# Optimization experiments

Hardware: AMD Instinct MI355X
Metric: run time of the kernel (lower is better)

The kernel has to match this reference:

```python
import jax, jax.numpy as jnp
import numpy as np

EPS = 1e-05
NUM_HEADS = 8
NUM_GROUPS = 32  # min(32, 512 // 4)


def setup_inputs() -> dict:
    key = jax.random.key(0)
    ks = jax.random.split(key, 5)
    B, C, T, X = 4, 512, 16, 2048
    return {
        "x": jax.random.normal(ks[0], (B, C, T, X), dtype=jnp.float32),
        "gn_w": jnp.ones((C,), dtype=jnp.float32),
        "gn_b": jnp.zeros((C,), dtype=jnp.float32),
        "qkv_w": jax.random.normal(ks[1], (3 * C, C), dtype=jnp.float32) * 0.02,
        "qkv_b": jax.random.normal(ks[2], (3 * C,), dtype=jnp.float32) * 0.02,
        "proj_w": jax.random.normal(ks[3], (C, C), dtype=jnp.float32) * 1e-5,
        "proj_b": jnp.zeros((C,), dtype=jnp.float32),
        "pos_emb": jax.random.normal(ks[4], (NUM_HEADS, 2 * T), dtype=jnp.float32) * 1e-5,
    }


def _group_norm(x, w, b):
    B, C, T, X = x.shape
    g = NUM_GROUPS
    xg = x.reshape(B, g, C // g, T, X)
    mu = xg.mean(axis=(2, 3, 4), keepdims=True)
    var = ((xg - mu) ** 2).mean(axis=(2, 3, 4), keepdims=True)
    xn = ((xg - mu) * jax.lax.rsqrt(var + EPS)).reshape(B, C, T, X)
    return xn * w[None, :, None, None] + b[None, :, None, None]


def reference(x, gn_w, gn_b, qkv_w, qkv_b, proj_w, proj_b, pos_emb):
    dtype = x.dtype
    x = x.astype(jnp.float32)
    B, C, T, X = x.shape
    H = NUM_HEADS
    hc = C // H

    xn = _group_norm(x, gn_w, gn_b)
    # 1x1 conv == channel matmul: [B, 3C, T, X]
    qkv = jnp.einsum('oc,bctx->botx', qkv_w, xn) + qkv_b[None, :, None, None]
    # 'b (n heads c) t x -> n (b x) heads t c'
    qkv = qkv.reshape(B, 3, H, hc, T, X)
    qkv = qkv.transpose(1, 0, 5, 2, 4, 3).reshape(3, B * X, H, T, hc)
    q, k, v = qkv[0], qkv[1], qkv[2]

    scale = 1.0 / np.sqrt(hc)
    attn = jnp.einsum('bhqc,bhkc->bhqk', q, k * scale)  # [(B X), H, T, T]

    i = jnp.arange(T)
    pairwise = i[:, None] - i[None, :] + T - 1        # [T, T] in [0, 2T-2]
    rel = pos_emb[:, pairwise]                         # [H, T, T]

    w = jax.nn.softmax(attn + rel[None], axis=-1)
    out = jnp.einsum('bhqk,bhkc->bhcq', w, v)          # [(B X), H, hc, T]
    # '(b x) h c t -> b (h c) t x'
    out = out.reshape(B, X, H, hc, T).transpose(0, 2, 3, 4, 1).reshape(B, C, T, X)

    y = jnp.einsum('oc,bctx->botx', proj_w, out) + proj_b[None, :, None, None]
    return y.astype(dtype)
```

## Files before the change

kernel.cpp:

```cpp
#include <hip/hip_runtime.h>
#include <math.h>

#define EPSV 1e-5f

typedef _Float16 f16;
typedef _Float16 f16x8 __attribute__((ext_vector_type(8)));
typedef _Float16 f16x4 __attribute__((ext_vector_type(4)));
typedef float f32x4 __attribute__((ext_vector_type(4)));

typedef const __attribute__((address_space(1))) void* as1_cvp;
typedef __attribute__((address_space(3))) void* as3_vp;
__device__ __forceinline__ void load_lds16(const void* g, void* l) {
    __builtin_amdgcn_global_load_lds((as1_cvp)g, (as3_vp)l, 16, 0, 0);
}

static constexpr int GROUP_N = 16 * 16 * 2048;

__global__ __launch_bounds__(256) void k_gn_part(const float* __restrict__ x,
                                                 float* __restrict__ psum,
                                                 float* __restrict__ psq) {
    const int blk = blockIdx.x;
    const int tid = threadIdx.x;
    const float* p = x + (size_t)blk * 32768;
    float s = 0.f, q = 0.f;
#pragma unroll
    for (int i = 0; i < 32; ++i) {
        float4 v = *(const float4*)(p + (size_t)(i * 256 + tid) * 4);
        s += v.x + v.y + v.z + v.w;
        q += v.x * v.x + v.y * v.y + v.z * v.z + v.w * v.w;
    }
#pragma unroll
    for (int off = 32; off > 0; off >>= 1) {
        s += __shfl_down(s, off);
        q += __shfl_down(q, off);
    }
    __shared__ float ls[4], lq[4];
    const int wave = tid >> 6, lane = tid & 63;
    if (lane == 0) { ls[wave] = s; lq[wave] = q; }
    __syncthreads();
    if (tid == 0) {
        psum[blk] = ls[0] + ls[1] + ls[2] + ls[3];
        psq[blk]  = lq[0] + lq[1] + lq[2] + lq[3];
    }
}

__global__ void k_gn_final(const float* __restrict__ psum, const float* __restrict__ psq,
                           float* __restrict__ mu, float* __restrict__ rs) {
    const int t = threadIdx.x;
    float s = 0.f, q = 0.f;
#pragma unroll
    for (int i = 0; i < 16; ++i) { s += psum[t * 16 + i]; q += psq[t * 16 + i]; }
    const float m = s / (float)GROUP_N;
    float v = q / (float)GROUP_N - m * m;
    mu[t] = m;
    rs[t] = 1.0f / sqrtf(v + EPSV);
}

__global__ __launch_bounds__(256) void k_fold_sc(const float* __restrict__ gn_w,
                                                 const float* __restrict__ gn_b,
                                                 const float* __restrict__ mu,
                                                 const float* __restrict__ rs,
                                                 float* __restrict__ sc,
                                                 float* __restrict__ beta) {
    const int u = blockIdx.x * 256 + threadIdx.x;
    const int b = u >> 9, c = u & 511;
    const int g = c >> 4;
    const float r = rs[b * 32 + g], m = mu[b * 32 + g];
    const float s = r * gn_w[c];
    sc[u]   = s;
    beta[u] = gn_b[c] - m * s;
}

__global__ __launch_bounds__(256) void k_fold_bias(const float* __restrict__ qkv_w,
                                                   const float* __restrict__ qkv_b,
                                                   const float* __restrict__ beta,
                                                   float* __restrict__ qbias) {
    const int u = blockIdx.x * 256 + threadIdx.x;
    const int b = u / 1536, o = u % 1536;
    float acc = qkv_b[o];
    const float* wr = qkv_w + (size_t)o * 512;
    const float* be = beta + b * 512;
#pragma unroll 4
    for (int c = 0; c < 512; c += 4) {
        float4 w4 = *(const float4*)(wr + c);
        float4 b4 = *(const float4*)(be + c);
        acc += w4.x * b4.x + w4.y * b4.y + w4.z * b4.z + w4.w * b4.w;
    }
    if (o >= 512 && o < 1024) acc *= 0.125f;
    qbias[u] = acc;
}


__global__ __launch_bounds__(256) void k_prep_w(const float* __restrict__ qkv_w,
                                                const float* __restrict__ proj_w,
                                                f16* __restrict__ w16,
                                                f16* __restrict__ p16) {
    const int id = blockIdx.x * 256 + threadIdx.x;
    if (id < 196608) {
        const int e0 = id * 4;
        const int o  = e0 >> 9;
        const float ksc = (o >= 512 && o < 1024) ? 0.125f : 1.0f;
        float4 v = *(const float4*)(qkv_w + e0);
        f16x4 h = { (f16)(v.x * ksc), (f16)(v.y * ksc), (f16)(v.z * ksc), (f16)(v.w * ksc) };
        *(f16x4*)(w16 + e0) = h;
    } else {
        const int e0 = (id - 196608) * 4;
        float4 v = *(const float4*)(proj_w + e0);
        f16x4 h = { (f16)v.x, (f16)v.y, (f16)v.z, (f16)v.w };
        *(f16x4*)(p16 + e0) = h;
    }
}

__global__ __launch_bounds__(256) void k_xt(const float* __restrict__ x,
                                            const float* __restrict__ sc,
                                            const float* __restrict__ beta,
                                            f16* __restrict__ xT) {
    const int x0 = blockIdx.x * 64;
    const int c0 = blockIdx.y * 64;
    const int b  = blockIdx.z >> 4, t = blockIdx.z & 15;
    const int tid = threadIdx.x;
    __shared__ float tile[64][68];
#pragma unroll
    for (int it = 0; it < 4; ++it) {
        int idx = it * 256 + tid;
        int c = idx >> 4, xq = idx & 15;
        int cg = c0 + c;
        float s = sc[b * 512 + cg], be = beta[b * 512 + cg];
        float4 v = *(const float4*)(x + (((size_t)(b * 512 + cg) * 16 + t) * 2048) + x0 + xq * 4);
        tile[c][xq * 4 + 0] = v.x * s + be;
        tile[c][xq * 4 + 1] = v.y * s + be;
        tile[c][xq * 4 + 2] = v.z * s + be;
        tile[c][xq * 4 + 3] = v.w * s + be;
    }
    __syncthreads();
#pragma unroll
    for (int it = 0; it < 2; ++it) {
        int idx = it * 256 + tid;
        int xr = idx >> 3, ch = idx & 7;
        f16x8 h;
#pragma unroll
        for (int e = 0; e < 8; ++e) h[e] = (f16)tile[ch * 8 + e][xr];
        *(f16x8*)(xT + (((size_t)(b * 2048 + x0 + xr) * 16 + t) * 512) + c0 + ch * 8) = h;
    }
}

__global__ __launch_bounds__(256) void k3_mfma(const f16* __restrict__ xT,
                                               const f16* __restrict__ w16,
                                               const float* __restrict__ qkv_b,
                                               const float* __restrict__ pos_emb,
                                               float* __restrict__ out,
                                               f16* __restrict__ aT) {
    extern __shared__ __attribute__((aligned(16))) char smem[];
    const int h  = blockIdx.x;
    const int x0 = blockIdx.y * 8;
    const int b  = blockIdx.z;
    const int tid = threadIdx.x;
    const int lane = tid & 63, w = tid >> 6;
    const int wm = w >> 1, wn = w & 1;
    const int t_l = lane & 15, g = lane >> 4;

    const f16* xTb = xT + ((size_t)b * 2048 + x0) * 16 * 512;

    const int l8 = lane >> 3;
    const int gc = (lane & 7) ^ l8;

    f32x4 acc[6][4];
#pragma unroll
    for (int mi = 0; mi < 6; ++mi)
#pragma unroll
        for (int ni = 0; ni < 4; ++ni) acc[mi][ni] = (f32x4){0.f, 0.f, 0.f, 0.f};

    {
#pragma unroll
        for (int i = 0; i < 6; ++i) {
            int m0 = (w * 6 + i) * 8;
            int m = m0 + l8;
            int o = (m >> 6) * 512 + h * 64 + (m & 63);
            load_lds16(w16 + (size_t)o * 512 + gc * 8, smem + m0 * 128);
        }
#pragma unroll
        for (int i = 0; i < 4; ++i) {
            int n0 = (w * 4 + i) * 8;
            int n = n0 + l8;
            load_lds16(xTb + (size_t)n * 512 + gc * 8, smem + 24576 + n0 * 128);
        }
    }
    __syncthreads();

    int cur = 0;
    for (int ks = 0; ks < 8; ++ks) {
        if (ks < 7) {
            char* bufn = smem + (cur ^ 1) * 40960;
            const int kon = (ks + 1) * 64;
#pragma unroll
            for (int i = 0; i < 6; ++i) {
                int m0 = (w * 6 + i) * 8;
                int m = m0 + l8;
                int o = (m >> 6) * 512 + h * 64 + (m & 63);
                load_lds16(w16 + (size_t)o * 512 + kon + gc * 8, bufn + m0 * 128);
            }
#pragma unroll
            for (int i = 0; i < 4; ++i) {
                int n0 = (w * 4 + i) * 8;
                int n = n0 + l8;
                load_lds16(xTb + (size_t)n * 512 + kon + gc * 8, bufn + 24576 + n0 * 128);
            }
        }
        const char* bufc = smem + cur * 40960;
        const f16* a_s = (const f16*)bufc;
        const f16* b_s = (const f16*)(bufc + 24576);
#pragma unroll
        for (int kk = 0; kk < 2; ++kk) {
            const int kb = kk * 4 + g;
            f16x8 af[6], bf[4];
#pragma unroll
            for (int mi = 0; mi < 6; ++mi) {
                int m = wm * 96 + mi * 16 + t_l;
                af[mi] = *(const f16x8*)(a_s + m * 64 + ((kb ^ (m & 7)) * 8));
            }
#pragma unroll
            for (int ni = 0; ni < 4; ++ni) {
                int n = wn * 64 + ni * 16 + t_l;
                bf[ni] = *(const f16x8*)(b_s + n * 64 + ((kb ^ (n & 7)) * 8));
            }
#pragma unroll
            for (int mi = 0; mi < 6; ++mi)
#pragma unroll
                for (int ni = 0; ni < 4; ++ni)
                    acc[mi][ni] = __builtin_amdgcn_mfma_f32_16x16x32_f16(af[mi], bf[ni], acc[mi][ni], 0, 0, 0);
        }
        __syncthreads();
        cur ^= 1;
    }

#pragma unroll
    for (int mi = 0; mi < 6; ++mi)
#pragma unroll
        for (int ni = 0; ni < 4; ++ni) {
            int n  = wn * 64 + ni * 16 + t_l;
            int mb = wm * 96 + mi * 16 + g * 4;
            int byte_off = n * 512 + (((mb >> 6) * 8 + (((mb >> 3) & 7) ^ (n & 7))) * 16) + (mb & 7) * 2;
            f16x4 hv;
#pragma unroll
            for (int r2 = 0; r2 < 4; ++r2) {
                int row = mb + r2;
                int reg = row >> 6;
                float qb = qkv_b[reg * 512 + h * 64 + (row & 63)];
                if (reg == 1) qb *= 0.125f;
                hv[r2] = (f16)(acc[mi][ni][r2] + qb);
            }
            *(f16x4*)(smem + byte_off) = hv;
        }
    __syncthreads();

#pragma unroll
    for (int xc = 0; xc < 2; ++xc) {
        const int xx = w * 2 + xc;
        const int nb = xx * 16;
        const int nrow = nb + t_l;
        const int rbase = nrow * 512;
        const int sw = nrow & 7;

        f32x4 s_acc = {0.f, 0.f, 0.f, 0.f};
#pragma unroll
        for (int half = 0; half < 2; ++half) {
            int qiA = (g + 4 * half) & 7;
            f16x8 afr = *(const f16x8*)(smem + rbase + ((8 + (qiA ^ sw)) * 16));
            f16x8 bfr = *(const f16x8*)(smem + rbase + ((qiA ^ sw) * 16));
            s_acc = __builtin_amdgcn_mfma_f32_16x16x32_f16(afr, bfr, s_acc, 0, 0, 0);
        }
        float sv[4];
#pragma unroll
        for (int r2 = 0; r2 < 4; ++r2)
            sv[r2] = s_acc[r2] + pos_emb[h * 32 + t_l - (g * 4 + r2) + 15];
        float mx = fmaxf(fmaxf(sv[0], sv[1]), fmaxf(sv[2], sv[3]));
        mx = fmaxf(mx, __shfl_xor(mx, 16));
        mx = fmaxf(mx, __shfl_xor(mx, 32));
        float es[4], ssum = 0.f;
#pragma unroll
        for (int r2 = 0; r2 < 4; ++r2) { es[r2] = __expf(sv[r2] - mx); ssum += es[r2]; }
        ssum += __shfl_xor(ssum, 16);
        ssum += __shfl_xor(ssum, 32);
        const float inv = 1.0f / ssum;
        f16x4 pfrag;
#pragma unroll
        for (int r2 = 0; r2 < 4; ++r2) pfrag[r2] = (f16)(es[r2] * inv);

        f32x4 o_acc[4];
#pragma unroll
        for (int cb = 0; cb < 4; ++cb) {
            int mV = 128 + cb * 16 + t_l;
            int qiV = (mV >> 3) & 7;
            f16x4 vfrag;
#pragma unroll
            for (int jj = 0; jj < 4; ++jj) {
                int nV = nb + g * 4 + jj;
                vfrag[jj] = *(const f16*)(smem + nV * 512 + ((16 + (qiV ^ (nV & 7))) * 16) + (mV & 7) * 2);
            }
            f32x4 z = {0.f, 0.f, 0.f, 0.f};
            o_acc[cb] = __builtin_amdgcn_mfma_f32_16x16x16f16(vfrag, pfrag, z, 0, 0, 0);
        }
        if (aT) {
            f16* dst = aT + (((size_t)(b * 2048 + x0 + xx) * 16) + t_l) * 512 + h * 64;
#pragma unroll
            for (int cb = 0; cb < 4; ++cb) {
                f16x4 hv;
#pragma unroll
                for (int r2 = 0; r2 < 4; ++r2) hv[r2] = (f16)o_acc[cb][r2];
                *(f16x4*)(dst + cb * 16 + g * 4) = hv;
            }
        } else {
#pragma unroll
            for (int cb = 0; cb < 4; ++cb) {
                int qd = cb * 4 + g;
                int byte_off = rbase + (((qd >> 3) * 8 + ((qd & 7) ^ sw)) * 16);
                *(f32x4*)(smem + byte_off) = o_acc[cb];
            }
        }
    }
    if (!aT) {
        __syncthreads();
        const int c = tid & 63, tq = tid >> 6;
        const int qc = c >> 2;
#pragma unroll
        for (int ti = 0; ti < 4; ++ti) {
            int t = tq * 4 + ti;
            float vals[8];
#pragma unroll
            for (int xx = 0; xx < 8; ++xx) {
                int n2 = xx * 16 + t;
                vals[xx] = *(const float*)(smem + n2 * 512 + (((qc >> 3) * 8 + ((qc & 7) ^ (n2 & 7))) * 16) + (c & 3) * 4);
            }
            float4 lo = {vals[0], vals[1], vals[2], vals[3]};
            float4 hi = {vals[4], vals[5], vals[6], vals[7]};
            size_t oaddr = (((size_t)b * 512 + h * 64 + c) * 16 + t) * 2048 + x0;
            *(float4*)(out + oaddr) = lo;
            *(float4*)(out + oaddr + 4) = hi;
        }
    }
}

__global__ __launch_bounds__(256) void k4x(const f16* __restrict__ attnT,
                                           const f16* __restrict__ p16,
                                           const float* __restrict__ pb,
                                           float* __restrict__ out) {
    extern __shared__ __attribute__((aligned(16))) char smem[];
    const int oc  = blockIdx.x;
    const int win = blockIdx.y;
    const int b   = blockIdx.z;
    const int tid = threadIdx.x;
    const int lane = tid & 63, w = tid >> 6;
    const int t_l = lane & 15, g = lane >> 4;
    const int l8 = lane >> 3;
    const int gc = (lane & 7) ^ l8;

    const f16* Bb = attnT + ((size_t)b * 2048 + win * 16) * 16 * 512;
    const f16* Ab = p16 + (size_t)oc * 64 * 512;

    f32x4 acc[4][4];
#pragma unroll
    for (int mi = 0; mi < 4; ++mi)
#pragma unroll
        for (int ni = 0; ni < 4; ++ni) acc[mi][ni] = (f32x4){0.f, 0.f, 0.f, 0.f};

    {
#pragma unroll
        for (int i = 0; i < 2; ++i) {
            int m0 = w * 16 + i * 8;
            load_lds16(Ab + (size_t)(m0 + l8) * 512 + gc * 8, smem + m0 * 128);
        }
#pragma unroll
        for (int i = 0; i < 8; ++i) {
            int n0 = w * 64 + i * 8;
            load_lds16(Bb + (size_t)(n0 + l8) * 512 + gc * 8, smem + 8192 + n0 * 128);
        }
    }
    __syncthreads();

    int cur = 0;
    for (int ks = 0; ks < 8; ++ks) {
        if (ks < 7) {
            char* bufn = smem + (cur ^ 1) * 40960;
            const int kon = (ks + 1) * 64;
#pragma unroll
            for (int i = 0; i < 2; ++i) {
                int m0 = w * 16 + i * 8;
                load_lds16(Ab + (size_t)(m0 + l8) * 512 + kon + gc * 8, bufn + m0 * 128);
            }
#pragma unroll
            for (int i = 0; i < 8; ++i) {
                int n0 = w * 64 + i * 8;
                load_lds16(Bb + (size_t)(n0 + l8) * 512 + kon + gc * 8, bufn + 8192 + n0 * 128);
            }
        }
        const char* bufc = smem + cur * 40960;
        const f16* a_s = (const f16*)bufc;
        const f16* b_s = (const f16*)(bufc + 8192);
#pragma unroll
        for (int kk = 0; kk < 2; ++kk) {
            const int kb = kk * 4 + g;
            f16x8 af[4], bf[4];
#pragma unroll
            for (int mi = 0; mi < 4; ++mi) {
                int m = mi * 16 + t_l;
                af[mi] = *(const f16x8*)(a_s + m * 64 + ((kb ^ (m & 7)) * 8));
            }
#pragma unroll
            for (int ni = 0; ni < 4; ++ni) {
                int n = w * 64 + ni * 16 + t_l;
                bf[ni] = *(const f16x8*)(b_s + n * 64 + ((kb ^ (n & 7)) * 8));
            }
#pragma unroll
            for (int mi = 0; mi < 4; ++mi)
#pragma unroll
                for (int ni = 0; ni < 4; ++ni)
                    acc[mi][ni] = __builtin_amdgcn_mfma_f32_16x16x32_f16(af[mi], bf[ni], acc[mi][ni], 0, 0, 0);
        }
        __syncthreads();
        cur ^= 1;
    }

    float* y_s = (float*)smem;
#pragma unroll
    for (int mi = 0; mi < 4; ++mi)
#pragma unroll
        for (int ni = 0; ni < 4; ++ni) {
            int nn = w * 64 + ni * 16 + t_l;
            int xx = nn >> 4, tt = nn & 15;
            int ob = mi * 16 + g * 4;
#pragma unroll
            for (int r2 = 0; r2 < 4; ++r2)
                y_s[(ob + r2) * 273 + xx * 17 + tt] = acc[mi][ni][r2];
        }
    __syncthreads();
#pragma unroll
    for (int k = 0; k < 4; ++k) {
        int pair = k * 256 + tid;
        int o = pair >> 4, t = pair & 15;
        float bias = pb[oc * 64 + o];
        float v[16];
#pragma unroll
        for (int xx = 0; xx < 16; ++xx) v[xx] = y_s[o * 273 + xx * 17 + t] + bias;
        size_t addr = (((size_t)b * 512 + oc * 64 + o) * 16 + t) * 2048 + win * 16;
#pragma unroll
        for (int v4 = 0; v4 < 4; ++v4) {
            float4 ov = {v[v4 * 4 + 0], v[v4 * 4 + 1], v[v4 * 4 + 2], v[v4 * 4 + 3]};
            *(float4*)(out + addr + v4 * 4) = ov;
        }
    }
}

__global__ __launch_bounds__(256) void k4_mfma(const f16* __restrict__ p16,
                                               const float* __restrict__ pb,
                                               float* __restrict__ io) {
    const int x0 = blockIdx.x * 64;
    const int t  = blockIdx.y;
    const int b  = blockIdx.z;
    const int tid = threadIdx.x, lane = tid & 63, w = tid >> 6;

    __shared__ __attribute__((aligned(16))) char smem4[81920];
    f16* in_sT = (f16*)smem4;
    f16* bp_s  = (f16*)(smem4 + 65536);

    const size_t base_in = (((size_t)b * 512) * 16 + t) * 2048 + x0;
#pragma unroll
    for (int it = 0; it < 32; ++it) {
        int s = it * 256 + tid;
        int c = s >> 4, xq = s & 15;
        float4 v = *(const float4*)(io + base_in + (size_t)c * 16 * 2048 + xq * 4);
        int kc = c >> 3, j = c & 7;
        float vv[4] = {v.x, v.y, v.z, v.w};
#pragma unroll
        for (int e = 0; e < 4; ++e) {
            int xx = xq * 4 + e;
            in_sT[xx * 512 + ((kc ^ (xx & 7)) * 8) + j] = (f16)vv[e];
        }
    }

    for (int no = 0; no < 4; ++no) {
        const int o_base = no * 128;
        f32x4 acc[4][2];
#pragma unroll
        for (int mi = 0; mi < 4; ++mi)
#pragma unroll
            for (int nj = 0; nj < 2; ++nj) acc[mi][nj] = (f32x4){0.f, 0.f, 0.f, 0.f};

        for (int ko = 0; ko < 8; ++ko) {
            __syncthreads();
#pragma unroll
            for (int it = 0; it < 4; ++it) {
                int s = it * 256 + tid;
                int orow = s >> 3, ch = s & 7;
                uint4 v = *(const uint4*)(p16 + (size_t)(o_base + orow) * 512 + ko * 64 + ch * 8);
                *(uint4*)(bp_s + orow * 64 + ((ch ^ (orow & 7)) * 8)) = v;
            }
            __syncthreads();
#pragma unroll
            for (int kk = 0; kk < 2; ++kk) {
                const int kb4 = kk * 4 + (lane >> 4);
                f16x8 af[4], bf[2];
#pragma unroll
                for (int mi = 0; mi < 4; ++mi) {
                    int xx = mi * 16 + (lane & 15);
                    int kc = ko * 8 + kb4;
                    af[mi] = *(const f16x8*)(in_sT + xx * 512 + ((kc ^ (xx & 7)) * 8));
                }
#pragma unroll
                for (int nj = 0; nj < 2; ++nj) {
                    int orow = w * 32 + nj * 16 + (lane & 15);
                    bf[nj] = *(const f16x8*)(bp_s + orow * 64 + ((kb4 ^ (orow & 7)) * 8));
                }
#pragma unroll
                for (int mi = 0; mi < 4; ++mi)
#pragma unroll
                    for (int nj = 0; nj < 2; ++nj)
                        acc[mi][nj] = __builtin_amdgcn_mfma_f32_16x16x32_f16(af[mi], bf[nj], acc[mi][nj], 0, 0, 0);
            }
        }
#pragma unroll
        for (int mi = 0; mi < 4; ++mi)
#pragma unroll
            for (int nj = 0; nj < 2; ++nj) {
                int o = o_base + w * 32 + nj * 16 + (lane & 15);
                int xxb = mi * 16 + (lane >> 4) * 4;
                float bias = pb[o];
                float4 ov = {acc[mi][nj][0] + bias, acc[mi][nj][1] + bias,
                             acc[mi][nj][2] + bias, acc[mi][nj][3] + bias};
                *(float4*)(io + (((size_t)b * 512 + o) * 16 + t) * 2048 + x0 + xxb) = ov;
            }
    }
}


__global__ __launch_bounds__(256) void k_qkv_attn(const float* __restrict__ x,
                                                  const float* __restrict__ qkv_w,
                                                  const float* __restrict__ sc,
                                                  const float* __restrict__ qbias,
                                                  const float* __restrict__ pos_emb,
                                                  float* __restrict__ out) {
    const int h  = blockIdx.x;
    const int x0 = blockIdx.y * 4;
    const int b  = blockIdx.z;
    const int tid = threadIdx.x;

    __shared__ float a_s[192][68];
    __shared__ float b_s[64][68];
    __shared__ float w_s[4][16][17];

    const int ty = tid >> 3;
    const int tx = tid & 7;

    float acc[6][8];
#pragma unroll
    for (int j = 0; j < 6; ++j)
#pragma unroll
        for (int k = 0; k < 8; ++k) acc[j][k] = 0.f;

    for (int ko = 0; ko < 512; ko += 64) {
        __syncthreads();
#pragma unroll
        for (int it = 0; it < 12; ++it) {
            int idx = it * 256 + tid;
            int m = idx >> 4;
            int c4 = (idx & 15) * 4;
            int g = m >> 6, i = m & 63;
            int o = g * 512 + h * 64 + i;
            float4 w4 = *(const float4*)(qkv_w + (size_t)o * 512 + ko + c4);
            float4 s4 = *(const float4*)(sc + b * 512 + ko + c4);
            float ksc = (g == 1) ? 0.125f : 1.0f;
            float4 v;
            v.x = w4.x * s4.x * ksc; v.y = w4.y * s4.y * ksc;
            v.z = w4.z * s4.z * ksc; v.w = w4.w * s4.w * ksc;
            *(float4*)&a_s[m][c4] = v;
        }
#pragma unroll
        for (int it = 0; it < 4; ++it) {
            int idx = it * 256 + tid;
            int cc = idx >> 4, t = idx & 15;
            float4 v = *(const float4*)(x + ((size_t)((b * 512 + ko + cc) * 16 + t)) * 2048 + x0);
            *(float4*)&b_s[cc][t * 4] = v;
        }
        __syncthreads();
#pragma unroll 4
        for (int cc = 0; cc < 64; ++cc) {
            float av[6];
#pragma unroll
            for (int j = 0; j < 6; ++j) av[j] = a_s[ty * 6 + j][cc];
            float4 b0 = *(const float4*)&b_s[cc][tx * 8];
            float4 b1 = *(const float4*)&b_s[cc][tx * 8 + 4];
            float bv[8] = {b0.x, b0.y, b0.z, b0.w, b1.x, b1.y, b1.z, b1.w};
#pragma unroll
            for (int j = 0; j < 6; ++j)
#pragma unroll
                for (int k = 0; k < 8; ++k)
                    acc[j][k] = fmaf(av[j], bv[k], acc[j][k]);
        }
    }
#pragma unroll
    for (int j = 0; j < 6; ++j) {
        int m = ty * 6 + j;
        int o = (m >> 6) * 512 + h * 64 + (m & 63);
        float qb = qbias[b * 1536 + o];
#pragma unroll
        for (int k = 0; k < 8; ++k) acc[j][k] += qb;
    }
    __syncthreads();
#pragma unroll
    for (int j = 0; j < 6; ++j)
#pragma unroll
        for (int k = 0; k < 8; ++k)
            a_s[ty * 6 + j][tx * 8 + k] = acc[j][k];
    __syncthreads();

    {
        const int xx = tid >> 6;
        const int t  = (tid >> 2) & 15;
        const int uq = tid & 3;
        float l[4] = {0.f, 0.f, 0.f, 0.f};
        for (int i = 0; i < 64; ++i) {
            float qv = a_s[i][t * 4 + xx];
#pragma unroll
            for (int uu = 0; uu < 4; ++uu)
                l[uu] = fmaf(qv, a_s[64 + i][(uq * 4 + uu) * 4 + xx], l[uu]);
        }
#pragma unroll
        for (int uu = 0; uu < 4; ++uu) {
            int u = uq * 4 + uu;
            w_s[xx][t][u] = l[uu] + pos_emb[h * 32 + t - u + 15];
        }
    }
    __syncthreads();
    if (tid < 64) {
        const int xx = tid >> 4, t = tid & 15;
        float mx = -3.4e38f;
#pragma unroll
        for (int u = 0; u < 16; ++u) mx = fmaxf(mx, w_s[xx][t][u]);
        float ssum = 0.f;
#pragma unroll
        for (int u = 0; u < 16; ++u) {
            float e = __expf(w_s[xx][t][u] - mx);
            w_s[xx][t][u] = e;
            ssum += e;
        }
        float inv = 1.0f / ssum;
#pragma unroll
        for (int u = 0; u < 16; ++u) w_s[xx][t][u] *= inv;
    }
    __syncthreads();
    {
        const int i  = tid & 63;
        const int t4 = tid >> 6;
        float4 varr[16];
#pragma unroll
        for (int u = 0; u < 16; ++u) varr[u] = *(const float4*)&a_s[128 + i][u * 4];
#pragma unroll
        for (int tt = 0; tt < 4; ++tt) {
            int t = t4 * 4 + tt;
            float4 o4 = {0.f, 0.f, 0.f, 0.f};
#pragma unroll
            for (int u = 0; u < 16; ++u) {
                o4.x = fmaf(w_s[0][t][u], varr[u].x, o4.x);
                o4.y = fmaf(w_s[1][t][u], varr[u].y, o4.y);
                o4.z = fmaf(w_s[2][t][u], varr[u].z, o4.z);
                o4.w = fmaf(w_s[3][t][u], varr[u].w, o4.w);
            }
            *(float4*)(out + ((size_t)((b * 512 + h * 64 + i) * 16 + t)) * 2048 + x0) = o4;
        }
    }
}

__global__ __launch_bounds__(256) void k_proj(const float* __restrict__ pw,
                                              const float* __restrict__ pb,
                                              float* __restrict__ io) {
    const int n0 = blockIdx.x * 32;
    const int b  = blockIdx.y;
    const int tid = threadIdx.x;
    __shared__ float in_s[512][36];
    __shared__ float w_s[128][65];

    {
        const float* src = io + (size_t)b * 512 * 32768 + n0;
#pragma unroll
        for (int it = 0; it < 64; ++it) {
            int idx = it * 256 + tid;
            int r = idx >> 5, j = idx & 31;
            in_s[r][j] = src[(size_t)r * 32768 + j];
        }
    }
    __syncthreads();

    const int ty = tid >> 3;
    const int tx = tid & 7;

    for (int mo = 0; mo < 512; mo += 128) {
        float acc[4][4];
#pragma unroll
        for (int j = 0; j < 4; ++j)
#pragma unroll
            for (int k = 0; k < 4; ++k) acc[j][k] = 0.f;

        for (int ko = 0; ko < 512; ko += 64) {
#pragma unroll
            for (int it = 0; it < 32; ++it) {
                int idx = it * 256 + tid;
                int m = idx >> 6, cc = idx & 63;
                w_s[m][cc] = pw[(size_t)(mo + m) * 512 + ko + cc];
            }
            __syncthreads();
#pragma unroll 4
            for (int cc = 0; cc < 64; ++cc) {
                float4 bv = *(const float4*)&in_s[ko + cc][tx * 4];
                float a0 = w_s[ty * 4 + 0][cc];
                float a1 = w_s[ty * 4 + 1][cc];
                float a2 = w_s[ty * 4 + 2][cc];
                float a3 = w_s[ty * 4 + 3][cc];
                acc[0][0] = fmaf(a0, bv.x, acc[0][0]); acc[0][1] = fmaf(a0, bv.y, acc[0][1]);
                acc[0][2] = fmaf(a0, bv.z, acc[0][2]); acc[0][3] = fmaf(a0, bv.w, acc[0][3]);
                acc[1][0] = fmaf(a1, bv.x, acc[1][0]); acc[1][1] = fmaf(a1, bv.y, acc[1][1]);
                acc[1][2] = fmaf(a1, bv.z, acc[1][2]); acc[1][3] = fmaf(a1, bv.w, acc[1][3]);
                acc[2][0] = fmaf(a2, bv.x, acc[2][0]); acc[2][1] = fmaf(a2, bv.y, acc[2][1]);
                acc[2][2] = fmaf(a2, bv.z, acc[2][2]); acc[2][3] = fmaf(a2, bv.w, acc[2][3]);
                acc[3][0] = fmaf(a3, bv.x, acc[3][0]); acc[3][1] = fmaf(a3, bv.y, acc[3][1]);
                acc[3][2] = fmaf(a3, bv.z, acc[3][2]); acc[3][3] = fmaf(a3, bv.w, acc[3][3]);
            }
            __syncthreads();
        }
#pragma unroll
        for (int j = 0; j < 4; ++j) {
            int m = mo + ty * 4 + j;
            float bias = pb[m];
            float4 o4 = {acc[j][0] + bias, acc[j][1] + bias, acc[j][2] + bias, acc[j][3] + bias};
            *(float4*)(io + (size_t)(b * 512 + m) * 32768 + n0 + tx * 4) = o4;
        }
    }
}

extern "C" void kernel_launch(void* const* d_in, const int* in_sizes, int n_in,
                              void* d_out, int out_size, void* d_ws, size_t ws_size,
                              hipStream_t stream) {
    (void)in_sizes; (void)n_in; (void)out_size;
    const float* x       = (const float*)d_in[0];
    const float* gn_w    = (const float*)d_in[1];
    const float* gn_b    = (const float*)d_in[2];
    const float* qkv_w   = (const float*)d_in[3];
    const float* qkv_b   = (const float*)d_in[4];
    const float* proj_w  = (const float*)d_in[5];
    const float* proj_b  = (const float*)d_in[6];
    const float* pos_emb = (const float*)d_in[7];
    float* out = (float*)d_out;

    float* ws    = (float*)d_ws;
    float* psum  = ws;
    float* psq   = ws + 2048;
    float* mu    = ws + 4096;
    float* rs    = ws + 4224;
    float* sc    = ws + 4352;
    float* beta  = ws + 6400;
    float* qbias = ws + 8448;

    const size_t W16_OFF = 65536;
    const size_t P16_OFF = W16_OFF + (size_t)1536 * 512 * 2;
    const size_t XT_OFF  = P16_OFF + (size_t)512 * 512 * 2;
    const size_t AT_OFF  = XT_OFF + (size_t)4 * 2048 * 16 * 512 * 2;
    const size_t NEEDED  = AT_OFF;
    const size_t NEEDED2 = AT_OFF + (size_t)4 * 2048 * 16 * 512 * 2;

    k_gn_part<<<dim3(2048), dim3(256), 0, stream>>>(x, psum, psq);
    k_gn_final<<<dim3(1), dim3(128), 0, stream>>>(psum, psq, mu, rs);
    k_fold_sc<<<dim3(8), dim3(256), 0, stream>>>(gn_w, gn_b, mu, rs, sc, beta);

    const int K3_LDS = 81920;
    hipError_t a1 = hipFuncSetAttribute((const void*)k3_mfma,
                                        hipFuncAttributeMaxDynamicSharedMemorySize, K3_LDS);
    hipError_t a2 = hipFuncSetAttribute((const void*)k4x,
                                        hipFuncAttributeMaxDynamicSharedMemorySize, K3_LDS);

    if (ws_size >= NEEDED && a1 == hipSuccess) {
        f16* w16 = (f16*)((char*)d_ws + W16_OFF);
        f16* p16 = (f16*)((char*)d_ws + P16_OFF);
        f16* xT  = (f16*)((char*)d_ws + XT_OFF);
        k_prep_w<<<dim3(1024), dim3(256), 0, stream>>>(qkv_w, proj_w, w16, p16);
        k_xt<<<dim3(32, 8, 64), dim3(256), 0, stream>>>(x, sc, beta, xT);
        if (ws_size >= NEEDED2 && a2 == hipSuccess) {
            f16* attnT = (f16*)((char*)d_ws + AT_OFF);
            k3_mfma<<<dim3(8, 256, 4), dim3(256), K3_LDS, stream>>>(xT, w16, qkv_b, pos_emb, out, attnT);
            k4x<<<dim3(8, 128, 4), dim3(256), K3_LDS, stream>>>(attnT, p16, proj_b, out);
        } else {
            k3_mfma<<<dim3(8, 256, 4), dim3(256), K3_LDS, stream>>>(xT, w16, qkv_b, pos_emb, out, nullptr);
            k4_mfma<<<dim3(32, 16, 4), dim3(256), 0, stream>>>(p16, proj_b, out);
        }
    } else {
        k_fold_bias<<<dim3(24), dim3(256), 0, stream>>>(qkv_w, qkv_b, beta, qbias);
        k_qkv_attn<<<dim3(8, 512, 4), dim3(256), 0, stream>>>(x, qkv_w, sc, qbias, pos_emb, out);
        k_proj<<<dim3(1024, 4), dim3(256), 0, stream>>>(proj_w, proj_b, out);
    }
}
```

Baseline: 614.0 us.

## Replace LDS-staged double-buffered GEMM loads with direct global-to-register MFMA operand loads

Both the QKV GEMM kernel and the projection kernel drop the global_load_lds double-buffered staging and instead have each lane read its f16x8 MFMA fragments directly from global memory, with the k loop unrolled by 2. k3 switches to a static 64KB shared array, since LDS is still needed for its epilogue, and no longer requests 80KB of dynamic LDS. The aim is to remove LDS traffic and barrier stalls and to raise occupancy. The cost is more redundant global and L2 reads, because fragments are no longer shared across waves, and loads that are only 16 bytes per lane with a 1KB row stride.

```diff
diff --git a/kernel.cpp b/kernel.cpp
--- a/kernel.cpp
+++ b/kernel.cpp
@@ -7,12 +7,6 @@
 typedef _Float16 f16x8 __attribute__((ext_vector_type(8)));
 typedef _Float16 f16x4 __attribute__((ext_vector_type(4)));
 typedef float f32x4 __attribute__((ext_vector_type(4)));
-
-typedef const __attribute__((address_space(1))) void* as1_cvp;
-typedef __attribute__((address_space(3))) void* as3_vp;
-__device__ __forceinline__ void load_lds16(const void* g, void* l) {
-    __builtin_amdgcn_global_load_lds((as1_cvp)g, (as3_vp)l, 16, 0, 0);
-}
 
 static constexpr int GROUP_N = 16 * 16 * 2048;
 
@@ -150,7 +144,7 @@
                                                const float* __restrict__ pos_emb,
                                                float* __restrict__ out,
                                                f16* __restrict__ aT) {
-    extern __shared__ __attribute__((aligned(16))) char smem[];
+    __shared__ __attribute__((aligned(16))) char smem[65536];
     const int h  = blockIdx.x;
     const int x0 = blockIdx.y * 8;
     const int b  = blockIdx.z;
@@ -161,8 +155,18 @@
 
     const f16* xTb = xT + ((size_t)b * 2048 + x0) * 16 * 512;
 
-    const int l8 = lane >> 3;
-    const int gc = (lane & 7) ^ l8;
+    int aoff[6], boff[4];
+#pragma unroll
+    for (int mi = 0; mi < 6; ++mi) {
+        int m = wm * 96 + mi * 16 + t_l;
+        int o = (m >> 6) * 512 + h * 64 + (m & 63);
+        aoff[mi] = o * 512 + g * 8;
+    }
+#pragma unroll
+    for (int ni = 0; ni < 4; ++ni) {
+        int n = wn * 64 + ni * 16 + t_l;
+        boff[ni] = n * 512 + g * 8;
+    }
 
     f32x4 acc[6][4];
 #pragma unroll
@@ -170,67 +174,19 @@
 #pragma unroll
         for (int ni = 0; ni < 4; ++ni) acc[mi][ni] = (f32x4){0.f, 0.f, 0.f, 0.f};
 
-    {
-#pragma unroll
-        for (int i = 0; i < 6; ++i) {
-            int m0 = (w * 6 + i) * 8;
-            int m = m0 + l8;
-            int o = (m >> 6) * 512 + h * 64 + (m & 63);
-            load_lds16(w16 + (size_t)o * 512 + gc * 8, smem + m0 * 128);
-        }
-#pragma unroll
-        for (int i = 0; i < 4; ++i) {
-            int n0 = (w * 4 + i) * 8;
-            int n = n0 + l8;
-            load_lds16(xTb + (size_t)n * 512 + gc * 8, smem + 24576 + n0 * 128);
-        }
-    }
-    __syncthreads();
-
-    int cur = 0;
-    for (int ks = 0; ks < 8; ++ks) {
-        if (ks < 7) {
-            char* bufn = smem + (cur ^ 1) * 40960;
-            const int kon = (ks + 1) * 64;
-#pragma unroll
-            for (int i = 0; i < 6; ++i) {
-                int m0 = (w * 6 + i) * 8;
-                int m = m0 + l8;
-                int o = (m >> 6) * 512 + h * 64 + (m & 63);
-                load_lds16(w16 + (size_t)o * 512 + kon + gc * 8, bufn + m0 * 128);
-            }
-#pragma unroll
-            for (int i = 0; i < 4; ++i) {
-                int n0 = (w * 4 + i) * 8;
-                int n = n0 + l8;
-                load_lds16(xTb + (size_t)n * 512 + kon + gc * 8, bufn + 24576 + n0 * 128);
-            }
-        }
-        const char* bufc = smem + cur * 40960;
-        const f16* a_s = (const f16*)bufc;
-        const f16* b_s = (const f16*)(bufc + 24576);
-#pragma unroll
-        for (int kk = 0; kk < 2; ++kk) {
-            const int kb = kk * 4 + g;
-            f16x8 af[6], bf[4];
-#pragma unroll
-            for (int mi = 0; mi < 6; ++mi) {
-                int m = wm * 96 + mi * 16 + t_l;
-                af[mi] = *(const f16x8*)(a_s + m * 64 + ((kb ^ (m & 7)) * 8));
-            }
-#pragma unroll
-            for (int ni = 0; ni < 4; ++ni) {
-                int n = wn * 64 + ni * 16 + t_l;
-                bf[ni] = *(const f16x8*)(b_s + n * 64 + ((kb ^ (n & 7)) * 8));
-            }
-#pragma unroll
-            for (int mi = 0; mi < 6; ++mi)
-#pragma unroll
-                for (int ni = 0; ni < 4; ++ni)
-                    acc[mi][ni] = __builtin_amdgcn_mfma_f32_16x16x32_f16(af[mi], bf[ni], acc[mi][ni], 0, 0, 0);
-        }
-        __syncthreads();
-        cur ^= 1;
+#pragma unroll 2
+    for (int kc = 0; kc < 16; ++kc) {
+        const int kof = kc * 32;
+        f16x8 af[6], bf[4];
+#pragma unroll
+        for (int mi = 0; mi < 6; ++mi) af[mi] = *(const f16x8*)(w16 + aoff[mi] + kof);
+#pragma unroll
+        for (int ni = 0; ni < 4; ++ni) bf[ni] = *(const f16x8*)(xTb + boff[ni] + kof);
+#pragma unroll
+        for (int mi = 0; mi < 6; ++mi)
+#pragma unroll
+            for (int ni = 0; ni < 4; ++ni)
+                acc[mi][ni] = __builtin_amdgcn_mfma_f32_16x16x32_f16(af[mi], bf[ni], acc[mi][ni], 0, 0, 0);
     }
 
 #pragma unroll
@@ -351,73 +307,35 @@
     const int tid = threadIdx.x;
     const int lane = tid & 63, w = tid >> 6;
     const int t_l = lane & 15, g = lane >> 4;
-    const int l8 = lane >> 3;
-    const int gc = (lane & 7) ^ l8;
 
     const f16* Bb = attnT + ((size_t)b * 2048 + win * 16) * 16 * 512;
     const f16* Ab = p16 + (size_t)oc * 64 * 512;
 
+    int aoff[4], boff[4];
+#pragma unroll
+    for (int mi = 0; mi < 4; ++mi) aoff[mi] = (mi * 16 + t_l) * 512 + g * 8;
+#pragma unroll
+    for (int ni = 0; ni < 4; ++ni) boff[ni] = (w * 64 + ni * 16 + t_l) * 512 + g * 8;
+
     f32x4 acc[4][4];
 #pragma unroll
     for (int mi = 0; mi < 4; ++mi)
 #pragma unroll
         for (int ni = 0; ni < 4; ++ni) acc[mi][ni] = (f32x4){0.f, 0.f, 0.f, 0.f};
 
-    {
-#pragma unroll
-        for (int i = 0; i < 2; ++i) {
-            int m0 = w * 16 + i * 8;
-            load_lds16(Ab + (size_t)(m0 + l8) * 512 + gc * 8, smem + m0 * 128);
-        }
-#pragma unroll
-        for (int i = 0; i < 8; ++i) {
-            int n0 = w * 64 + i * 8;
-            load_lds16(Bb + (size_t)(n0 + l8) * 512 + gc * 8, smem + 8192 + n0 * 128);
-        }
-    }
-    __syncthreads();
-
-    int cur = 0;
-    for (int ks = 0; ks < 8; ++ks) {
-        if (ks < 7) {
-            char* bufn = smem + (cur ^ 1) * 40960;
-            const int kon = (ks + 1) * 64;
-#pragma unroll
-            for (int i = 0; i < 2; ++i) {
-                int m0 = w * 16 + i * 8;
-                load_lds16(Ab + (size_t)(m0 + l8) * 512 + kon + gc * 8, bufn + m0 * 128);
-            }
-#pragma unroll
-            for (int i = 0; i < 8; ++i) {
-                int n0 = w * 64 + i * 8;
-                load_lds16(Bb + (size_t)(n0 + l8) * 512 + kon + gc * 8, bufn + 8192 + n0 * 128);
-            }
-        }
-        const char* bufc = smem + cur * 40960;
-        const f16* a_s = (const f16*)bufc;
-        const f16* b_s = (const f16*)(bufc + 8192);
-#pragma unroll
-        for (int kk = 0; kk < 2; ++kk) {
-            const int kb = kk * 4 + g;
-            f16x8 af[4], bf[4];
-#pragma unroll
-            for (int mi = 0; mi < 4; ++mi) {
-                int m = mi * 16 + t_l;
-                af[mi] = *(const f16x8*)(a_s + m * 64 + ((kb ^ (m & 7)) * 8));
-            }
-#pragma unroll
-            for (int ni = 0; ni < 4; ++ni) {
-                int n = w * 64 + ni * 16 + t_l;
-                bf[ni] = *(const f16x8*)(b_s + n * 64 + ((kb ^ (n & 7)) * 8));
-            }
-#pragma unroll
-            for (int mi = 0; mi < 4; ++mi)
-#pragma unroll
-                for (int ni = 0; ni < 4; ++ni)
-                    acc[mi][ni] = __builtin_amdgcn_mfma_f32_16x16x32_f16(af[mi], bf[ni], acc[mi][ni], 0, 0, 0);
-        }
-        __syncthreads();
-        cur ^= 1;
+#pragma unroll 2
+    for (int kc = 0; kc < 16; ++kc) {
+        const int kof = kc * 32;
+        f16x8 af[4], bf[4];
+#pragma unroll
+        for (int mi = 0; mi < 4; ++mi) af[mi] = *(const f16x8*)(Ab + aoff[mi] + kof);
+#pragma unroll
+        for (int ni = 0; ni < 4; ++ni) bf[ni] = *(const f16x8*)(Bb + boff[ni] + kof);
+#pragma unroll
+        for (int mi = 0; mi < 4; ++mi)
+#pragma unroll
+            for (int ni = 0; ni < 4; ++ni)
+                acc[mi][ni] = __builtin_amdgcn_mfma_f32_16x16x32_f16(af[mi], bf[ni], acc[mi][ni], 0, 0, 0);
     }
 
     float* y_s = (float*)smem;
@@ -769,13 +687,11 @@
     k_gn_final<<<dim3(1), dim3(128), 0, stream>>>(psum, psq, mu, rs);
     k_fold_sc<<<dim3(8), dim3(256), 0, stream>>>(gn_w, gn_b, mu, rs, sc, beta);
 
-    const int K3_LDS = 81920;
-    hipError_t a1 = hipFuncSetAttribute((const void*)k3_mfma,
-                                        hipFuncAttributeMaxDynamicSharedMemorySize, K3_LDS);
+    const int K4_LDS = 81920;
     hipError_t a2 = hipFuncSetAttribute((const void*)k4x,
-                                        hipFuncAttributeMaxDynamicSharedMemorySize, K3_LDS);
-
-    if (ws_size >= NEEDED && a1 == hipSuccess) {
+                                        hipFuncAttributeMaxDynamicSharedMemorySize, K4_LDS);
+
+    if (ws_size >= NEEDED) {
         f16* w16 = (f16*)((char*)d_ws + W16_OFF);
         f16* p16 = (f16*)((char*)d_ws + P16_OFF);
         f16* xT  = (f16*)((char*)d_ws + XT_OFF);
@@ -783,10 +699,10 @@
         k_xt<<<dim3(32, 8, 64), dim3(256), 0, stream>>>(x, sc, beta, xT);
         if (ws_size >= NEEDED2 && a2 == hipSuccess) {
             f16* attnT = (f16*)((char*)d_ws + AT_OFF);
-            k3_mfma<<<dim3(8, 256, 4), dim3(256), K3_LDS, stream>>>(xT, w16, qkv_b, pos_emb, out, attnT);
-            k4x<<<dim3(8, 128, 4), dim3(256), K3_LDS, stream>>>(attnT, p16, proj_b, out);
+            k3_mfma<<<dim3(8, 256, 4), dim3(256), 0, stream>>>(xT, w16, qkv_b, pos_emb, out, attnT);
+            k4x<<<dim3(8, 128, 4), dim3(256), K4_LDS, stream>>>(attnT, p16, proj_b, out);
         } else {
-            k3_mfma<<<dim3(8, 256, 4), dim3(256), K3_LDS, stream>>>(xT, w16, qkv_b, pos_emb, out, nullptr);
+            k3_mfma<<<dim3(8, 256, 4), dim3(256), 0, stream>>>(xT, w16, qkv_b, pos_emb, out, nullptr);
             k4_mfma<<<dim3(32, 16, 4), dim3(256), 0, stream>>>(p16, proj_b, out);
         }
     } else {
```

Result: slower. 1.097 ms (+78.6%).

## Fuse group-norm statistics into transpose pass and fold norm scale into per-batch weights

Applied to the files above, without the earlier changes.

The separate group-norm statistics pass over x is removed. A new transpose kernel converts raw x to fp16 layout and emits per-tile partial sums in the same read. The per-channel norm scale is folded into a per-batch fp16 copy of the QKV weights, and the norm shift into a per-batch bias, so the GEMM consumes un-normalized x. This saves one full read of the 256MB input, at the cost of per-batch weight copies and storing un-normalized activations in fp16, which could lose precision.

```diff
diff --git a/kernel.cpp b/kernel.cpp
--- a/kernel.cpp
+++ b/kernel.cpp
@@ -15,6 +15,76 @@
 }
 
 static constexpr int GROUP_N = 16 * 16 * 2048;
+
+__global__ __launch_bounds__(256) void k_xtstat(const float* __restrict__ x,
+                                                f16* __restrict__ xT,
+                                                float* __restrict__ psum2,
+                                                float* __restrict__ psq2) {
+    const int x0 = blockIdx.x * 64;
+    const int c0 = blockIdx.y * 64;
+    const int b  = blockIdx.z >> 4, t = blockIdx.z & 15;
+    const int tid = threadIdx.x;
+    __shared__ float tile[64][68];
+#pragma unroll
+    for (int it = 0; it < 4; ++it) {
+        int idx = it * 256 + tid;
+        int c = idx >> 4, xq = idx & 15;
+        float4 v = *(const float4*)(x + (((size_t)(b * 512 + c0 + c) * 16 + t) * 2048) + x0 + xq * 4);
+        tile[c][xq * 4 + 0] = v.x;
+        tile[c][xq * 4 + 1] = v.y;
+        tile[c][xq * 4 + 2] = v.z;
+        tile[c][xq * 4 + 3] = v.w;
+    }
+    __syncthreads();
+#pragma unroll
+    for (int it = 0; it < 2; ++it) {
+        int idx = it * 256 + tid;
+        int xr = idx >> 3, ch = idx & 7;
+        f16x8 h;
+#pragma unroll
+        for (int e = 0; e < 8; ++e) h[e] = (f16)tile[ch * 8 + e][xr];
+        *(f16x8*)(xT + (((size_t)(b * 2048 + x0 + xr) * 16 + t) * 512) + c0 + ch * 8) = h;
+    }
+    {
+        const int gg = tid >> 6, lane = tid & 63;
+        float s = 0.f, q = 0.f;
+#pragma unroll
+        for (int i = 0; i < 16; ++i) {
+            float v = tile[gg * 16 + i][lane];
+            s += v; q += v * v;
+        }
+#pragma unroll
+        for (int off = 32; off > 0; off >>= 1) {
+            s += __shfl_down(s, off);
+            q += __shfl_down(q, off);
+        }
+        if (lane == 0) {
+            int grp = b * 32 + blockIdx.y * 4 + gg;
+            int col = blockIdx.x * 16 + t;
+            psum2[grp * 512 + col] = s;
+            psq2[grp * 512 + col] = q;
+        }
+    }
+}
+
+__global__ void k_gn_final2(const float* __restrict__ psum2, const float* __restrict__ psq2,
+                            float* __restrict__ mu, float* __restrict__ rs) {
+    const int t = threadIdx.x;
+    float s = 0.f, q = 0.f;
+    const float* ps = psum2 + t * 512;
+    const float* pq = psq2 + t * 512;
+#pragma unroll 4
+    for (int i = 0; i < 512; i += 4) {
+        float4 a = *(const float4*)(ps + i);
+        float4 c = *(const float4*)(pq + i);
+        s += a.x + a.y + a.z + a.w;
+        q += c.x + c.y + c.z + c.w;
+    }
+    const float m = s / (float)GROUP_N;
+    float v = q / (float)GROUP_N - m * m;
+    mu[t] = m;
+    rs[t] = 1.0f / sqrtf(v + EPSV);
+}
 
 __global__ __launch_bounds__(256) void k_gn_part(const float* __restrict__ x,
                                                  float* __restrict__ psum,
@@ -90,6 +160,29 @@
     qbias[u] = acc;
 }
 
+__global__ __launch_bounds__(256) void k_prep_wb(const float* __restrict__ qkv_w,
+                                                 const float* __restrict__ sc,
+                                                 f16* __restrict__ w16b) {
+    const int id = blockIdx.x * 256 + threadIdx.x;
+    const int b  = blockIdx.y;
+    const int e0 = id * 4;
+    const int o  = e0 >> 9;
+    const float ksc = (o >= 512 && o < 1024) ? 0.125f : 1.0f;
+    float4 wv = *(const float4*)(qkv_w + e0);
+    float4 s4 = *(const float4*)(sc + b * 512 + (e0 & 511));
+    f16x4 h = { (f16)(wv.x * s4.x * ksc), (f16)(wv.y * s4.y * ksc),
+                (f16)(wv.z * s4.z * ksc), (f16)(wv.w * s4.w * ksc) };
+    *(f16x4*)(w16b + (size_t)b * 786432 + e0) = h;
+}
+
+__global__ __launch_bounds__(256) void k_prep_p(const float* __restrict__ proj_w,
+                                                f16* __restrict__ p16) {
+    const int id = blockIdx.x * 256 + threadIdx.x;
+    const int e0 = id * 4;
+    float4 v = *(const float4*)(proj_w + e0);
+    f16x4 h = { (f16)v.x, (f16)v.y, (f16)v.z, (f16)v.w };
+    *(f16x4*)(p16 + e0) = h;
+}
 
 __global__ __launch_bounds__(256) void k_prep_w(const float* __restrict__ qkv_w,
                                                 const float* __restrict__ proj_w,
@@ -145,8 +238,10 @@
 }
 
 __global__ __launch_bounds__(256) void k3_mfma(const f16* __restrict__ xT,
-                                               const f16* __restrict__ w16,
+                                               const f16* __restrict__ wsrc,
+                                               size_t w_bstride,
                                                const float* __restrict__ qkv_b,
+                                               const float* __restrict__ qb_full,
                                                const float* __restrict__ pos_emb,
                                                float* __restrict__ out,
                                                f16* __restrict__ aT) {
@@ -160,6 +255,7 @@
     const int t_l = lane & 15, g = lane >> 4;
 
     const f16* xTb = xT + ((size_t)b * 2048 + x0) * 16 * 512;
+    const f16* Wb  = wsrc + (size_t)b * w_bstride;
 
     const int l8 = lane >> 3;
     const int gc = (lane & 7) ^ l8;
@@ -176,7 +272,7 @@
             int m0 = (w * 6 + i) * 8;
             int m = m0 + l8;
             int o = (m >> 6) * 512 + h * 64 + (m & 63);
-            load_lds16(w16 + (size_t)o * 512 + gc * 8, smem + m0 * 128);
+            load_lds16(Wb + (size_t)o * 512 + gc * 8, smem + m0 * 128);
         }
 #pragma unroll
         for (int i = 0; i < 4; ++i) {
@@ -197,7 +293,7 @@
                 int m0 = (w * 6 + i) * 8;
                 int m = m0 + l8;
                 int o = (m >> 6) * 512 + h * 64 + (m & 63);
-                load_lds16(w16 + (size_t)o * 512 + kon + gc * 8, bufn + m0 * 128);
+                load_lds16(Wb + (size_t)o * 512 + kon + gc * 8, bufn + m0 * 128);
             }
 #pragma unroll
             for (int i = 0; i < 4; ++i) {
@@ -233,24 +329,43 @@
         cur ^= 1;
     }
 
-#pragma unroll
-    for (int mi = 0; mi < 6; ++mi)
-#pragma unroll
-        for (int ni = 0; ni < 4; ++ni) {
-            int n  = wn * 64 + ni * 16 + t_l;
-            int mb = wm * 96 + mi * 16 + g * 4;
-            int byte_off = n * 512 + (((mb >> 6) * 8 + (((mb >> 3) & 7) ^ (n & 7))) * 16) + (mb & 7) * 2;
-            f16x4 hv;
-#pragma unroll
-            for (int r2 = 0; r2 < 4; ++r2) {
-                int row = mb + r2;
-                int reg = row >> 6;
-                float qb = qkv_b[reg * 512 + h * 64 + (row & 63)];
-                if (reg == 1) qb *= 0.125f;
-                hv[r2] = (f16)(acc[mi][ni][r2] + qb);
-            }
-            *(f16x4*)(smem + byte_off) = hv;
-        }
+    if (qb_full) {
+        const float* qb = qb_full + b * 1536;
+#pragma unroll
+        for (int mi = 0; mi < 6; ++mi)
+#pragma unroll
+            for (int ni = 0; ni < 4; ++ni) {
+                int n  = wn * 64 + ni * 16 + t_l;
+                int mb = wm * 96 + mi * 16 + g * 4;
+                int byte_off = n * 512 + (((mb >> 6) * 8 + (((mb >> 3) & 7) ^ (n & 7))) * 16) + (mb & 7) * 2;
+                f16x4 hv;
+#pragma unroll
+                for (int r2 = 0; r2 < 4; ++r2) {
+                    int row = mb + r2;
+                    hv[r2] = (f16)(acc[mi][ni][r2] + qb[(row >> 6) * 512 + h * 64 + (row & 63)]);
+                }
+                *(f16x4*)(smem + byte_off) = hv;
+            }
+    } else {
+#pragma unroll
+        for (int mi = 0; mi < 6; ++mi)
+#pragma unroll
+            for (int ni = 0; ni < 4; ++ni) {
+                int n  = wn * 64 + ni * 16 + t_l;
+                int mb = wm * 96 + mi * 16 + g * 4;
+                int byte_off = n * 512 + (((mb >> 6) * 8 + (((mb >> 3) & 7) ^ (n & 7))) * 16) + (mb & 7) * 2;
+                f16x4 hv;
+#pragma unroll
+                for (int r2 = 0; r2 < 4; ++r2) {
+                    int row = mb + r2;
+                    int reg = row >> 6;
+                    float qb = qkv_b[reg * 512 + h * 64 + (row & 63)];
+                    if (reg == 1) qb *= 0.125f;
+                    hv[r2] = (f16)(acc[mi][ni][r2] + qb);
+                }
+                *(f16x4*)(smem + byte_off) = hv;
+            }
+    }
     __syncthreads();
 
 #pragma unroll
@@ -293,9 +408,9 @@
             int qiV = (mV >> 3) & 7;
             f16x4 vfrag;
 #pragma unroll
-            for (int jj = 0; jj < 4; ++jj) {
-                int nV = nb + g * 4 + jj;
-                vfrag[jj] = *(const f16*)(smem + nV * 512 + ((16 + (qiV ^ (nV & 7))) * 16) + (mV & 7) * 2);
+            for (int jj2 = 0; jj2 < 4; ++jj2) {
+                int nV = nb + g * 4 + jj2;
+                vfrag[jj2] = *(const f16*)(smem + nV * 512 + ((16 + (qiV ^ (nV & 7))) * 16) + (mV & 7) * 2);
             }
             f32x4 z = {0.f, 0.f, 0.f, 0.f};
             o_acc[cb] = __builtin_amdgcn_mfma_f32_16x16x16f16(vfrag, pfrag, z, 0, 0, 0);
@@ -447,87 +562,6 @@
             float4 ov = {v[v4 * 4 + 0], v[v4 * 4 + 1], v[v4 * 4 + 2], v[v4 * 4 + 3]};
             *(float4*)(out + addr + v4 * 4) = ov;
         }
-    }
-}
-
-__global__ __launch_bounds__(256) void k4_mfma(const f16* __restrict__ p16,
-                                               const float* __restrict__ pb,
-                                               float* __restrict__ io) {
-    const int x0 = blockIdx.x * 64;
-    const int t  = blockIdx.y;
-    const int b  = blockIdx.z;
-    const int tid = threadIdx.x, lane = tid & 63, w = tid >> 6;
-
-    __shared__ __attribute__((aligned(16))) char smem4[81920];
-    f16* in_sT = (f16*)smem4;
-    f16* bp_s  = (f16*)(smem4 + 65536);
-
-    const size_t base_in = (((size_t)b * 512) * 16 + t) * 2048 + x0;
-#pragma unroll
-    for (int it = 0; it < 32; ++it) {
-        int s = it * 256 + tid;
-        int c = s >> 4, xq = s & 15;
-        float4 v = *(const float4*)(io + base_in + (size_t)c * 16 * 2048 + xq * 4);
-        int kc = c >> 3, j = c & 7;
-        float vv[4] = {v.x, v.y, v.z, v.w};
-#pragma unroll
-        for (int e = 0; e < 4; ++e) {
-            int xx = xq * 4 + e;
-            in_sT[xx * 512 + ((kc ^ (xx & 7)) * 8) + j] = (f16)vv[e];
-        }
-    }
-
-    for (int no = 0; no < 4; ++no) {
-        const int o_base = no * 128;
-        f32x4 acc[4][2];
-#pragma unroll
-        for (int mi = 0; mi < 4; ++mi)
-#pragma unroll
-            for (int nj = 0; nj < 2; ++nj) acc[mi][nj] = (f32x4){0.f, 0.f, 0.f, 0.f};
-
-        for (int ko = 0; ko < 8; ++ko) {
-            __syncthreads();
-#pragma unroll
-            for (int it = 0; it < 4; ++it) {
-                int s = it * 256 + tid;
-                int orow = s >> 3, ch = s & 7;
-                uint4 v = *(const uint4*)(p16 + (size_t)(o_base + orow) * 512 + ko * 64 + ch * 8);
-                *(uint4*)(bp_s + orow * 64 + ((ch ^ (orow & 7)) * 8)) = v;
-            }
-            __syncthreads();
-#pragma unroll
-            for (int kk = 0; kk < 2; ++kk) {
-                const int kb4 = kk * 4 + (lane >> 4);
-                f16x8 af[4], bf[2];
-#pragma unroll
-                for (int mi = 0; mi < 4; ++mi) {
-                    int xx = mi * 16 + (lane & 15);
-                    int kc = ko * 8 + kb4;
-                    af[mi] = *(const f16x8*)(in_sT + xx * 512 + ((kc ^ (xx & 7)) * 8));
-                }
-#pragma unroll
-                for (int nj = 0; nj < 2; ++nj) {
-                    int orow = w * 32 + nj * 16 + (lane & 15);
-                    bf[nj] = *(const f16x8*)(bp_s + orow * 64 + ((kb4 ^ (orow & 7)) * 8));
-                }
-#pragma unroll
-                for (int mi = 0; mi < 4; ++mi)
-#pragma unroll
-                    for (int nj = 0; nj < 2; ++nj)
-                        acc[mi][nj] = __builtin_amdgcn_mfma_f32_16x16x32_f16(af[mi], bf[nj], acc[mi][nj], 0, 0, 0);
-            }
-        }
-#pragma unroll
-        for (int mi = 0; mi < 4; ++mi)
-#pragma unroll
-            for (int nj = 0; nj < 2; ++nj) {
-                int o = o_base + w * 32 + nj * 16 + (lane & 15);
-                int xxb = mi * 16 + (lane >> 4) * 4;
-                float bias = pb[o];
-                float4 ov = {acc[mi][nj][0] + bias, acc[mi][nj][1] + bias,
-                             acc[mi][nj][2] + bias, acc[mi][nj][3] + bias};
-                *(float4*)(io + (((size_t)b * 512 + o) * 16 + t) * 2048 + x0 + xxb) = ov;
-            }
     }
 }
 
@@ -758,38 +792,59 @@
     float* beta  = ws + 6400;
     float* qbias = ws + 8448;
 
+    const size_t XT_BYTES = (size_t)4 * 2048 * 16 * 512 * 2;
+
+    const size_t W16B_OFF = 65536;
+    const size_t P16B_OFF = W16B_OFF + (size_t)4 * 1536 * 512 * 2;
+    const size_t XT1_OFF  = P16B_OFF + (size_t)512 * 512 * 2;
+    const size_t AT1_OFF  = XT1_OFF + XT_BYTES;
+    const size_t NEED_T1  = AT1_OFF + XT_BYTES;
+
     const size_t W16_OFF = 65536;
     const size_t P16_OFF = W16_OFF + (size_t)1536 * 512 * 2;
-    const size_t XT_OFF  = P16_OFF + (size_t)512 * 512 * 2;
-    const size_t AT_OFF  = XT_OFF + (size_t)4 * 2048 * 16 * 512 * 2;
-    const size_t NEEDED  = AT_OFF;
-    const size_t NEEDED2 = AT_OFF + (size_t)4 * 2048 * 16 * 512 * 2;
-
-    k_gn_part<<<dim3(2048), dim3(256), 0, stream>>>(x, psum, psq);
-    k_gn_final<<<dim3(1), dim3(128), 0, stream>>>(psum, psq, mu, rs);
-    k_fold_sc<<<dim3(8), dim3(256), 0, stream>>>(gn_w, gn_b, mu, rs, sc, beta);
-
-    const int K3_LDS = 81920;
+    const size_t XT2_OFF = P16_OFF + (size_t)512 * 512 * 2;
+    const size_t AT2_OFF = XT2_OFF + XT_BYTES;
+    const size_t NEED_T2 = AT2_OFF + XT_BYTES;
+
+    const int K_LDS = 81920;
     hipError_t a1 = hipFuncSetAttribute((const void*)k3_mfma,
-                                        hipFuncAttributeMaxDynamicSharedMemorySize, K3_LDS);
+                                        hipFuncAttributeMaxDynamicSharedMemorySize, K_LDS);
     hipError_t a2 = hipFuncSetAttribute((const void*)k4x,
-                                        hipFuncAttributeMaxDynamicSharedMemorySize, K3_LDS);
-
-    if (ws_size >= NEEDED && a1 == hipSuccess) {
-        f16* w16 = (f16*)((char*)d_ws + W16_OFF);
-        f16* p16 = (f16*)((char*)d_ws + P16_OFF);
-        f16* xT  = (f16*)((char*)d_ws + XT_OFF);
+                                        hipFuncAttributeMaxDynamicSharedMemorySize, K_LDS);
+
+    if (ws_size >= NEED_T1 && a1 == hipSuccess && a2 == hipSuccess) {
+        f16* w16b  = (f16*)((char*)d_ws + W16B_OFF);
+        f16* p16   = (f16*)((char*)d_ws + P16B_OFF);
+        f16* xT    = (f16*)((char*)d_ws + XT1_OFF);
+        f16* attnT = (f16*)((char*)d_ws + AT1_OFF);
+        float* psum2 = (float*)((char*)d_ws + AT1_OFF);
+        float* psq2  = (float*)((char*)d_ws + AT1_OFF + 262144);
+        k_xtstat<<<dim3(32, 8, 64), dim3(256), 0, stream>>>(x, xT, psum2, psq2);
+        k_gn_final2<<<dim3(1), dim3(128), 0, stream>>>(psum2, psq2, mu, rs);
+        k_fold_sc<<<dim3(8), dim3(256), 0, stream>>>(gn_w, gn_b, mu, rs, sc, beta);
+        k_fold_bias<<<dim3(24), dim3(256), 0, stream>>>(qkv_w, qkv_b, beta, qbias);
+        k_prep_wb<<<dim3(768, 4), dim3(256), 0, stream>>>(qkv_w, sc, w16b);
+        k_prep_p<<<dim3(256), dim3(256), 0, stream>>>(proj_w, p16);
+        k3_mfma<<<dim3(8, 256, 4), dim3(256), K_LDS, stream>>>(xT, w16b, (size_t)786432,
+                                                               qkv_b, qbias, pos_emb, out, attnT);
+        k4x<<<dim3(8, 128, 4), dim3(256), K_LDS, stream>>>(attnT, p16, proj_b, out);
+    } else if (ws_size >= NEED_T2 && a1 == hipSuccess && a2 == hipSuccess) {
+        f16* w16   = (f16*)((char*)d_ws + W16_OFF);
+        f16* p16   = (f16*)((char*)d_ws + P16_OFF);
+        f16* xT    = (f16*)((char*)d_ws + XT2_OFF);
+        f16* attnT = (f16*)((char*)d_ws + AT2_OFF);
+        k_gn_part<<<dim3(2048), dim3(256), 0, stream>>>(x, psum, psq);
+        k_gn_final<<<dim3(1), dim3(128), 0, stream>>>(psum, psq, mu, rs);
+        k_fold_sc<<<dim3(8), dim3(256), 0, stream>>>(gn_w, gn_b, mu, rs, sc, beta);
         k_prep_w<<<dim3(1024), dim3(256), 0, stream>>>(qkv_w, proj_w, w16, p16);
         k_xt<<<dim3(32, 8, 64), dim3(256), 0, stream>>>(x, sc, beta, xT);
-        if (ws_size >= NEEDED2 && a2 == hipSuccess) {
-            f16* attnT = (f16*)((char*)d_ws + AT_OFF);
-            k3_mfma<<<dim3(8, 256, 4), dim3(256), K3_LDS, stream>>>(xT, w16, qkv_b, pos_emb, out, attnT);
-            k4x<<<dim3(8, 128, 4), dim3(256), K3_LDS, stream>>>(attnT, p16, proj_b, out);
-        } else {
-            k3_mfma<<<dim3(8, 256, 4), dim3(256), K3_LDS, stream>>>(xT, w16, qkv_b, pos_emb, out, nullptr);
-            k4_mfma<<<dim3(32, 16, 4), dim3(256), 0, stream>>>(p16, proj_b, out);
-        }
+        k3_mfma<<<dim3(8, 256, 4), dim3(256), K_LDS, stream>>>(xT, w16, (size_t)0,
+                                                               qkv_b, nullptr, pos_emb, out, attnT);
+        k4x<<<dim3(8, 128, 4), dim3(256), K_LDS, stream>>>(attnT, p16, proj_b, out);
     } else {
+        k_gn_part<<<dim3(2048), dim3(256), 0, stream>>>(x, psum, psq);
+        k_gn_final<<<dim3(1), dim3(128), 0, stream>>>(psum, psq, mu, rs);
+        k_fold_sc<<<dim3(8), dim3(256), 0, stream>>>(gn_w, gn_b, mu, rs, sc, beta);
         k_fold_bias<<<dim3(24), dim3(256), 0, stream>>>(qkv_w, qkv_b, beta, qbias);
         k_qkv_attn<<<dim3(8, 512, 4), dim3(256), 0, stream>>>(x, qkv_w, sc, qbias, pos_emb, out);
         k_proj<<<dim3(1024, 4), dim3(256), 0, stream>>>(proj_w, proj_b, out);
```

Result: no change. 609.5 us (-0.7%).
